# Performance work log

Measured on AMD Instinct MI355X. Metric: run time of the kernel, lower is better.

Reference implementation:

```python
import jax, jax.numpy as jnp
import numpy as np

NUM_NODES = 100000
NUM_EDGES = 640000
D_IN = 128
D_OUT = 128


def setup_inputs() -> dict:
    key = jax.random.key(0)
    k_x, k_s, k_t, k_w, k_lin = jax.random.split(key, 5)
    x = jax.random.normal(k_x, (NUM_NODES, D_IN), dtype=jnp.float32)
    source = jax.random.randint(k_s, (NUM_EDGES,), 0, NUM_NODES, dtype=jnp.int32)
    target = jax.random.randint(k_t, (NUM_EDGES,), 0, NUM_NODES, dtype=jnp.int32)
    edge_weights = jax.random.uniform(k_w, (NUM_EDGES,), dtype=jnp.float32)
    # nn.Linear weight, shape (out, in), kaiming-uniform-ish init
    bound = 1.0 / np.sqrt(D_IN)
    W = jax.random.uniform(k_lin, (D_OUT, D_IN), dtype=jnp.float32, minval=-bound, maxval=bound)
    return {"x": x, "W": W, "edge_weights": edge_weights, "source": source, "target": target}


def reference(x, W, edge_weights, source, target):
    # LinearMessageCreator: project all nodes first (as in the torch code), then gather per edge
    h = jnp.einsum("nd,od->no", x, W)            # (num_nodes, d_out)
    msg = h[source] * edge_weights[:, None]       # (num_edges, d_out)
    # SumAggregator: scatter-add messages into target nodes
    delta = jax.ops.segment_sum(msg, target, num_segments=x.shape[0])
    # OnlyUpdate: return aggregated messages
    return delta
```

## Files before the change

### kernel.cpp

```cpp
#include <hip/hip_runtime.h>
#include <hip/hip_bf16.h>

#define NN 100000
#define NE 640000
#define D 128

#define SCAN_CHUNK 1024
#define NBLK ((NN + SCAN_CHUNK - 1) / SCAN_CHUNK)

#define OFF_COUNTS  0u
#define OFF_OFFSETS 400000u
#define OFF_CURSOR  800016u
#define OFF_BSUM    1200016u
#define OFF_BSUMEX  1200528u
#define OFF_PSRC    1201040u
#define OFF_PW      3761040u
#define WS_NEED     6321040u

__global__ __launch_bounds__(256) void k_hist(const int* __restrict__ tgt,
                                              int* __restrict__ counts) {
    int e = blockIdx.x * 256 + threadIdx.x;
    if (e < NE) atomicAdd(&counts[tgt[e]], 1);
}

__global__ __launch_bounds__(256) void k_scan_part(const int* __restrict__ counts,
                                                   int* __restrict__ bsum) {
    __shared__ int sd[256];
    int b = blockIdx.x, t = threadIdx.x;
    int base = b * SCAN_CHUNK + t * 4;
    int s = 0;
    #pragma unroll
    for (int k = 0; k < 4; ++k) { int i = base + k; s += (i < NN) ? counts[i] : 0; }
    sd[t] = s; __syncthreads();
    for (int off = 128; off > 0; off >>= 1) {
        if (t < off) sd[t] += sd[t + off];
        __syncthreads();
    }
    if (t == 0) bsum[b] = sd[0];
}

__global__ __launch_bounds__(128) void k_scan_mid(const int* __restrict__ bsum,
                                                  int* __restrict__ bsumex,
                                                  int* __restrict__ offsets) {
    __shared__ int sd[128];
    int t = threadIdx.x;
    int v = (t < NBLK) ? bsum[t] : 0;
    sd[t] = v; __syncthreads();
    for (int off = 1; off < 128; off <<= 1) {
        int tmp = (t >= off) ? sd[t - off] : 0;
        __syncthreads();
        sd[t] += tmp;
        __syncthreads();
    }
    if (t < NBLK) bsumex[t] = sd[t] - v;
    if (t == 0) offsets[NN] = NE;
}

__global__ __launch_bounds__(256) void k_scan_final(const int* __restrict__ counts,
                                                    const int* __restrict__ bsumex,
                                                    int* __restrict__ offsets,
                                                    int* __restrict__ cursor) {
    __shared__ int sd[256];
    int b = blockIdx.x, t = threadIdx.x;
    int base = b * SCAN_CHUNK + t * 4;
    int c[4]; int s = 0;
    #pragma unroll
    for (int k = 0; k < 4; ++k) { int i = base + k; c[k] = (i < NN) ? counts[i] : 0; s += c[k]; }
    sd[t] = s; __syncthreads();
    for (int off = 1; off < 256; off <<= 1) {
        int tmp = (t >= off) ? sd[t - off] : 0;
        __syncthreads();
        sd[t] += tmp;
        __syncthreads();
    }
    int run = sd[t] - s + bsumex[b];
    #pragma unroll
    for (int k = 0; k < 4; ++k) {
        int i = base + k;
        if (i < NN) { offsets[i] = run; cursor[i] = run; }
        run += c[k];
    }
}

__global__ __launch_bounds__(256) void k_fill(const int* __restrict__ src,
                                              const int* __restrict__ tgt,
                                              const float* __restrict__ ew,
                                              int* __restrict__ cursor,
                                              int* __restrict__ psrc,
                                              float* __restrict__ pw) {
    int e = blockIdx.x * 256 + threadIdx.x;
    if (e < NE) {
        int t = tgt[e];
        int p = atomicAdd(&cursor[t], 1);
        psrc[p] = src[e];
        pw[p] = ew[e];
    }
}

__global__ __launch_bounds__(256) void k_gather(const float* __restrict__ x,
                                                const int* __restrict__ offsets,
                                                const int* __restrict__ psrc,
                                                const float* __restrict__ pw,
                                                float* __restrict__ out) {
    int wid = blockIdx.x * 4 + (threadIdx.x >> 6);
    int lane = threadIdx.x & 63;
    if (wid >= NN) return;
    int beg = offsets[wid], end = offsets[wid + 1];
    const float2* x2 = (const float2*)x;
    float a0 = 0.f, a1 = 0.f;
    int s = 0; float w = 0.f;
    if (beg < end) { s = psrc[beg]; w = pw[beg]; }
    for (int i = beg; i < end; ++i) {
        int sn = 0; float wn = 0.f;
        if (i + 1 < end) { sn = psrc[i + 1]; wn = pw[i + 1]; }
        float2 v = x2[(size_t)s * 64 + lane];
        a0 = fmaf(v.x, w, a0);
        a1 = fmaf(v.y, w, a1);
        s = sn; w = wn;
    }
    ((float2*)out)[(size_t)wid * 64 + lane] = make_float2(a0, a1);
}

#define PBN 64

__device__ __forceinline__ float bflo(unsigned u) { return __uint_as_float(u << 16); }
__device__ __forceinline__ float bfhi(unsigned u) { return __uint_as_float(u & 0xffff0000u); }

__global__ __launch_bounds__(256) void k_project(const float* __restrict__ W,
                                                 float* __restrict__ io) {
    __shared__ __align__(16) float xs[PBN][D];
    __shared__ __align__(16) __hip_bfloat16 Wb[D][D];

    const int tid = threadIdx.x;

    const float4* W4 = (const float4*)W;
    for (int k = 0; k < 16; ++k) {
        int idx = k * 256 + tid;
        int f = idx & 127;
        int dq = idx >> 7;
        float4 v = W4[(size_t)f * 32 + dq];
        Wb[dq * 4 + 0][f] = __float2bfloat16(v.x);
        Wb[dq * 4 + 1][f] = __float2bfloat16(v.y);
        Wb[dq * 4 + 2][f] = __float2bfloat16(v.z);
        Wb[dq * 4 + 3][f] = __float2bfloat16(v.w);
    }

    const long nb = (long)blockIdx.x * PBN;
    const float4* io4 = (const float4*)io;
    for (int k = 0; k < 8; ++k) {
        int idx = k * 256 + tid;
        int n = idx >> 5;
        int dq = idx & 31;
        long node = nb + n;
        float4 v = (node < NN) ? io4[node * 32 + dq] : make_float4(0.f, 0.f, 0.f, 0.f);
        *(float4*)&xs[n][dq * 4] = v;
    }
    __syncthreads();

    const int fg = tid & 15;
    const int ng = tid >> 4;
    float acc[4][8];
    #pragma unroll
    for (int r = 0; r < 4; ++r)
        #pragma unroll
        for (int ff = 0; ff < 8; ++ff) acc[r][ff] = 0.f;

    for (int d = 0; d < D; d += 4) {
        float4 xv[4];
        #pragma unroll
        for (int r = 0; r < 4; ++r) xv[r] = *(const float4*)&xs[ng * 4 + r][d];
        #pragma unroll
        for (int j = 0; j < 4; ++j) {
            uint4 wv = *(const uint4*)&Wb[d + j][fg * 8];
            float wf0 = bflo(wv.x), wf1 = bfhi(wv.x);
            float wf2 = bflo(wv.y), wf3 = bfhi(wv.y);
            float wf4 = bflo(wv.z), wf5 = bfhi(wv.z);
            float wf6 = bflo(wv.w), wf7 = bfhi(wv.w);
            #pragma unroll
            for (int r = 0; r < 4; ++r) {
                float xj = ((const float*)&xv[r])[j];
                acc[r][0] = fmaf(xj, wf0, acc[r][0]);
                acc[r][1] = fmaf(xj, wf1, acc[r][1]);
                acc[r][2] = fmaf(xj, wf2, acc[r][2]);
                acc[r][3] = fmaf(xj, wf3, acc[r][3]);
                acc[r][4] = fmaf(xj, wf4, acc[r][4]);
                acc[r][5] = fmaf(xj, wf5, acc[r][5]);
                acc[r][6] = fmaf(xj, wf6, acc[r][6]);
                acc[r][7] = fmaf(xj, wf7, acc[r][7]);
            }
        }
    }

    #pragma unroll
    for (int r = 0; r < 4; ++r) {
        long node = nb + ng * 4 + r;
        if (node < NN) {
            float4* dst = (float4*)&io[node * D + fg * 8];
            dst[0] = make_float4(acc[r][0], acc[r][1], acc[r][2], acc[r][3]);
            dst[1] = make_float4(acc[r][4], acc[r][5], acc[r][6], acc[r][7]);
        }
    }
}

__global__ __launch_bounds__(256) void gcn_scatter(const float* __restrict__ x,
                                                   const float* __restrict__ ew,
                                                   const int* __restrict__ src,
                                                   const int* __restrict__ tgt,
                                                   float* __restrict__ out) {
    int tid = blockIdx.x * 256 + threadIdx.x;
    int e = tid >> 5;
    int t = tid & 31;
    if (e >= NE) return;
    int s = src[e];
    int g = tgt[e];
    float w = ew[e];
    float4 xv = reinterpret_cast<const float4*>(x)[s * 32 + t];
    float* dst = out + (size_t)g * D + (t << 2);
    atomicAdd(dst + 0, xv.x * w);
    atomicAdd(dst + 1, xv.y * w);
    atomicAdd(dst + 2, xv.z * w);
    atomicAdd(dst + 3, xv.w * w);
}

extern "C" void kernel_launch(void* const* d_in, const int* in_sizes, int n_in,
                              void* d_out, int out_size, void* d_ws, size_t ws_size,
                              hipStream_t stream) {
    const float* x   = (const float*)d_in[0];
    const float* W   = (const float*)d_in[1];
    const float* ew  = (const float*)d_in[2];
    const int*   src = (const int*)d_in[3];
    const int*   tgt = (const int*)d_in[4];
    float* out = (float*)d_out;

    if (ws_size >= WS_NEED) {
        char* ws = (char*)d_ws;
        int*   counts  = (int*)(ws + OFF_COUNTS);
        int*   offsets = (int*)(ws + OFF_OFFSETS);
        int*   cursor  = (int*)(ws + OFF_CURSOR);
        int*   bsum    = (int*)(ws + OFF_BSUM);
        int*   bsumex  = (int*)(ws + OFF_BSUMEX);
        int*   psrc    = (int*)(ws + OFF_PSRC);
        float* pw      = (float*)(ws + OFF_PW);

        hipMemsetAsync(counts, 0, (size_t)NN * sizeof(int), stream);
        k_hist<<<(NE + 255) / 256, 256, 0, stream>>>(tgt, counts);
        k_scan_part<<<NBLK, 256, 0, stream>>>(counts, bsum);
        k_scan_mid<<<1, 128, 0, stream>>>(bsum, bsumex, offsets);
        k_scan_final<<<NBLK, 256, 0, stream>>>(counts, bsumex, offsets, cursor);
        k_fill<<<(NE + 255) / 256, 256, 0, stream>>>(src, tgt, ew, cursor, psrc, pw);
        k_gather<<<(NN + 3) / 4, 256, 0, stream>>>(x, offsets, psrc, pw, out);
    } else {
        hipMemsetAsync(out, 0, (size_t)out_size * sizeof(float), stream);
        gcn_scatter<<<(NE * 32 + 255) / 256, 256, 0, stream>>>(x, ew, src, tgt, out);
    }

    k_project<<<(NN + PBN - 1) / PBN, 256, 0, stream>>>(W, out);
}
```

Measured before the change: 314.3 us.

## Gather from bf16 copy of x, pack edge pairs, single-block scan

Three changes at once. The three-kernel scan is replaced by one 1024-thread single-block scan. The separate source and weight arrays become one packed int2 per edge. When workspace allows, x is converted to bf16 so the random-row gather reads half the bytes. The conversion pass costs an extra full read and write of x, and bf16 rounding of x lowers accuracy. The single-block scan gives up parallelism in exchange for fewer launches.

Result: slower. 548.2 us (+74.4%).

```diff
diff --git a/kernel.cpp b/kernel.cpp
--- a/kernel.cpp
+++ b/kernel.cpp
@@ -5,17 +5,16 @@
 #define NE 640000
 #define D 128
 
-#define SCAN_CHUNK 1024
-#define NBLK ((NN + SCAN_CHUNK - 1) / SCAN_CHUNK)
-
 #define OFF_COUNTS  0u
 #define OFF_OFFSETS 400000u
 #define OFF_CURSOR  800016u
-#define OFF_BSUM    1200016u
-#define OFF_BSUMEX  1200528u
-#define OFF_PSRC    1201040u
-#define OFF_PW      3761040u
-#define WS_NEED     6321040u
+#define OFF_PE      1201040u
+#define WS_T2       6321040u
+#define OFF_XB      6321040u
+#define WS_FULL     31921040u
+
+__device__ __forceinline__ float bflo(unsigned u) { return __uint_as_float(u << 16); }
+__device__ __forceinline__ float bfhi(unsigned u) { return __uint_as_float(u & 0xffff0000u); }
 
 __global__ __launch_bounds__(256) void k_hist(const int* __restrict__ tgt,
                                               int* __restrict__ counts) {
@@ -23,108 +22,101 @@
     if (e < NE) atomicAdd(&counts[tgt[e]], 1);
 }
 
-__global__ __launch_bounds__(256) void k_scan_part(const int* __restrict__ counts,
-                                                   int* __restrict__ bsum) {
-    __shared__ int sd[256];
-    int b = blockIdx.x, t = threadIdx.x;
-    int base = b * SCAN_CHUNK + t * 4;
+#define SCAN_T 1024
+__global__ __launch_bounds__(1024) void k_scan_all(const int* __restrict__ counts,
+                                                   int* __restrict__ offsets,
+                                                   int* __restrict__ cursor) {
+    __shared__ int sd[SCAN_T];
+    const int t = threadIdx.x;
+    const int CH = (NN + SCAN_T - 1) / SCAN_T;
+    const int base = t * CH;
     int s = 0;
-    #pragma unroll
-    for (int k = 0; k < 4; ++k) { int i = base + k; s += (i < NN) ? counts[i] : 0; }
+    for (int k = 0; k < CH; ++k) { int i = base + k; if (i < NN) s += counts[i]; }
     sd[t] = s; __syncthreads();
-    for (int off = 128; off > 0; off >>= 1) {
-        if (t < off) sd[t] += sd[t + off];
-        __syncthreads();
-    }
-    if (t == 0) bsum[b] = sd[0];
-}
-
-__global__ __launch_bounds__(128) void k_scan_mid(const int* __restrict__ bsum,
-                                                  int* __restrict__ bsumex,
-                                                  int* __restrict__ offsets) {
-    __shared__ int sd[128];
-    int t = threadIdx.x;
-    int v = (t < NBLK) ? bsum[t] : 0;
-    sd[t] = v; __syncthreads();
-    for (int off = 1; off < 128; off <<= 1) {
+    for (int off = 1; off < SCAN_T; off <<= 1) {
         int tmp = (t >= off) ? sd[t - off] : 0;
         __syncthreads();
         sd[t] += tmp;
         __syncthreads();
     }
-    if (t < NBLK) bsumex[t] = sd[t] - v;
+    int run = sd[t] - s;
+    for (int k = 0; k < CH; ++k) {
+        int i = base + k;
+        if (i < NN) { int c = counts[i]; offsets[i] = run; cursor[i] = run; run += c; }
+    }
     if (t == 0) offsets[NN] = NE;
-}
-
-__global__ __launch_bounds__(256) void k_scan_final(const int* __restrict__ counts,
-                                                    const int* __restrict__ bsumex,
-                                                    int* __restrict__ offsets,
-                                                    int* __restrict__ cursor) {
-    __shared__ int sd[256];
-    int b = blockIdx.x, t = threadIdx.x;
-    int base = b * SCAN_CHUNK + t * 4;
-    int c[4]; int s = 0;
-    #pragma unroll
-    for (int k = 0; k < 4; ++k) { int i = base + k; c[k] = (i < NN) ? counts[i] : 0; s += c[k]; }
-    sd[t] = s; __syncthreads();
-    for (int off = 1; off < 256; off <<= 1) {
-        int tmp = (t >= off) ? sd[t - off] : 0;
-        __syncthreads();
-        sd[t] += tmp;
-        __syncthreads();
-    }
-    int run = sd[t] - s + bsumex[b];
-    #pragma unroll
-    for (int k = 0; k < 4; ++k) {
-        int i = base + k;
-        if (i < NN) { offsets[i] = run; cursor[i] = run; }
-        run += c[k];
-    }
 }
 
 __global__ __launch_bounds__(256) void k_fill(const int* __restrict__ src,
                                               const int* __restrict__ tgt,
                                               const float* __restrict__ ew,
                                               int* __restrict__ cursor,
-                                              int* __restrict__ psrc,
-                                              float* __restrict__ pw) {
+                                              int2* __restrict__ pe) {
     int e = blockIdx.x * 256 + threadIdx.x;
     if (e < NE) {
         int t = tgt[e];
         int p = atomicAdd(&cursor[t], 1);
-        psrc[p] = src[e];
-        pw[p] = ew[e];
-    }
-}
-
-__global__ __launch_bounds__(256) void k_gather(const float* __restrict__ x,
-                                                const int* __restrict__ offsets,
-                                                const int* __restrict__ psrc,
-                                                const float* __restrict__ pw,
-                                                float* __restrict__ out) {
+        pe[p] = make_int2(src[e], __float_as_int(ew[e]));
+    }
+}
+
+__global__ __launch_bounds__(256) void k_conv(const float* __restrict__ x,
+                                              unsigned* __restrict__ xb) {
+    int i = blockIdx.x * 256 + threadIdx.x;
+    if (i < NN * 64) {
+        float2 v = ((const float2*)x)[i];
+        __hip_bfloat16 b0 = __float2bfloat16(v.x);
+        __hip_bfloat16 b1 = __float2bfloat16(v.y);
+        unsigned u0 = *(const unsigned short*)&b0;
+        unsigned u1 = *(const unsigned short*)&b1;
+        xb[i] = u0 | (u1 << 16);
+    }
+}
+
+__global__ __launch_bounds__(256) void k_gather_bf(const unsigned* __restrict__ xb,
+                                                   const int* __restrict__ offsets,
+                                                   const int2* __restrict__ pe,
+                                                   float* __restrict__ out) {
+    int wid = blockIdx.x * 4 + (threadIdx.x >> 6);
+    int lane = threadIdx.x & 63;
+    if (wid >= NN) return;
+    int beg = offsets[wid], end = offsets[wid + 1];
+    float a0 = 0.f, a1 = 0.f;
+    int2 e = (beg < end) ? pe[beg] : make_int2(0, 0);
+    for (int i = beg; i < end; ++i) {
+        int2 en = (i + 1 < end) ? pe[i + 1] : make_int2(0, 0);
+        unsigned v = xb[(size_t)e.x * 64 + lane];
+        float w = __int_as_float(e.y);
+        a0 = fmaf(bflo(v), w, a0);
+        a1 = fmaf(bfhi(v), w, a1);
+        e = en;
+    }
+    ((float2*)out)[(size_t)wid * 64 + lane] = make_float2(a0, a1);
+}
+
+__global__ __launch_bounds__(256) void k_gather_f32(const float* __restrict__ x,
+                                                    const int* __restrict__ offsets,
+                                                    const int2* __restrict__ pe,
+                                                    float* __restrict__ out) {
     int wid = blockIdx.x * 4 + (threadIdx.x >> 6);
     int lane = threadIdx.x & 63;
     if (wid >= NN) return;
     int beg = offsets[wid], end = offsets[wid + 1];
     const float2* x2 = (const float2*)x;
     float a0 = 0.f, a1 = 0.f;
-    int s = 0; float w = 0.f;
-    if (beg < end) { s = psrc[beg]; w = pw[beg]; }
+    int2 e = (beg < end) ? pe[beg] : make_int2(0, 0);
     for (int i = beg; i < end; ++i) {
-        int sn = 0; float wn = 0.f;
-        if (i + 1 < end) { sn = psrc[i + 1]; wn = pw[i + 1]; }
-        float2 v = x2[(size_t)s * 64 + lane];
+        int2 en = (i + 1 < end) ? pe[i + 1] : make_int2(0, 0);
+        float2 v = x2[(size_t)e.x * 64 + lane];
+        float w = __int_as_float(e.y);
         a0 = fmaf(v.x, w, a0);
         a1 = fmaf(v.y, w, a1);
-        s = sn; w = wn;
+        e = en;
     }
     ((float2*)out)[(size_t)wid * 64 + lane] = make_float2(a0, a1);
 }
 
 #define PBN 64
-
-__device__ __forceinline__ float bflo(unsigned u) { return __uint_as_float(u << 16); }
-__device__ __forceinline__ float bfhi(unsigned u) { return __uint_as_float(u & 0xffff0000u); }
 
 __global__ __launch_bounds__(256) void k_project(const float* __restrict__ W,
                                                  float* __restrict__ io) {
@@ -232,23 +224,25 @@
     const int*   tgt = (const int*)d_in[4];
     float* out = (float*)d_out;
 
-    if (ws_size >= WS_NEED) {
+    if (ws_size >= WS_T2) {
         char* ws = (char*)d_ws;
-        int*   counts  = (int*)(ws + OFF_COUNTS);
-        int*   offsets = (int*)(ws + OFF_OFFSETS);
-        int*   cursor  = (int*)(ws + OFF_CURSOR);
-        int*   bsum    = (int*)(ws + OFF_BSUM);
-        int*   bsumex  = (int*)(ws + OFF_BSUMEX);
-        int*   psrc    = (int*)(ws + OFF_PSRC);
-        float* pw      = (float*)(ws + OFF_PW);
+        int*  counts  = (int*)(ws + OFF_COUNTS);
+        int*  offsets = (int*)(ws + OFF_OFFSETS);
+        int*  cursor  = (int*)(ws + OFF_CURSOR);
+        int2* pe      = (int2*)(ws + OFF_PE);
 
         hipMemsetAsync(counts, 0, (size_t)NN * sizeof(int), stream);
         k_hist<<<(NE + 255) / 256, 256, 0, stream>>>(tgt, counts);
-        k_scan_part<<<NBLK, 256, 0, stream>>>(counts, bsum);
-        k_scan_mid<<<1, 128, 0, stream>>>(bsum, bsumex, offsets);
-        k_scan_final<<<NBLK, 256, 0, stream>>>(counts, bsumex, offsets, cursor);
-        k_fill<<<(NE + 255) / 256, 256, 0, stream>>>(src, tgt, ew, cursor, psrc, pw);
-        k_gather<<<(NN + 3) / 4, 256, 0, stream>>>(x, offsets, psrc, pw, out);
+        k_scan_all<<<1, SCAN_T, 0, stream>>>(counts, offsets, cursor);
+        k_fill<<<(NE + 255) / 256, 256, 0, stream>>>(src, tgt, ew, cursor, pe);
+
+        if (ws_size >= WS_FULL) {
+            unsigned* xb = (unsigned*)(ws + OFF_XB);
+            k_conv<<<(NN * 64 + 255) / 256, 256, 0, stream>>>(x, xb);
+            k_gather_bf<<<(NN + 3) / 4, 256, 0, stream>>>(xb, offsets, pe, out);
+        } else {
+            k_gather_f32<<<(NN + 3) / 4, 256, 0, stream>>>(x, offsets, pe, out);
+        }
     } else {
         hipMemsetAsync(out, 0, (size_t)out_size * sizeof(float), stream);
         gcn_scatter<<<(NE * 32 + 255) / 256, 256, 0, stream>>>(x, ew, src, tgt, out);
```
